# Optimization experiments

Hardware: AMD Instinct MI355X
Metric: run time of the kernel (lower is better)

The kernel has to match this reference:

```python
import jax, jax.numpy as jnp
import numpy as np

N = 50000      # nodes
E = 800000     # edges
IN = 128       # in_channels
C = 32         # hidden_channels per head
H = 8          # heads
NC = 2         # num_classes
EPS = 1e-5     # batchnorm eps
SLOPE = 0.2    # leaky relu negative slope


def setup_inputs() -> dict:
    key = jax.random.key(0)
    ks = jax.random.split(key, 16)
    d = {}
    d["x"] = jax.random.normal(ks[0], (N, IN), dtype=jnp.float32)
    d["edge_index"] = jax.random.randint(ks[1], (2, E), 0, N, dtype=jnp.int64)
    # layer 0: IN -> H*C (concat)
    s0 = 1.0 / np.sqrt(IN)
    d["Wl0"] = jax.random.normal(ks[2], (IN, H * C), dtype=jnp.float32) * s0
    d["Wr0"] = jax.random.normal(ks[3], (IN, H * C), dtype=jnp.float32) * s0
    d["att0"] = jax.random.normal(ks[4], (H, C), dtype=jnp.float32) * (1.0 / np.sqrt(C))
    d["b0"] = jnp.zeros((H * C,), dtype=jnp.float32)
    d["g0"] = jnp.ones((H * C,), dtype=jnp.float32)
    d["be0"] = jnp.zeros((H * C,), dtype=jnp.float32)
    d["m0"] = jax.random.normal(ks[5], (H * C,), dtype=jnp.float32) * 0.1
    d["v0"] = jax.random.uniform(ks[6], (H * C,), dtype=jnp.float32, minval=0.5, maxval=1.5)
    # layer 1: H*C -> C (mean over heads, concat=False)
    s1 = 1.0 / np.sqrt(H * C)
    d["Wl1"] = jax.random.normal(ks[7], (H * C, H * C), dtype=jnp.float32) * s1
    d["Wr1"] = jax.random.normal(ks[8], (H * C, H * C), dtype=jnp.float32) * s1
    d["att1"] = jax.random.normal(ks[9], (H, C), dtype=jnp.float32) * (1.0 / np.sqrt(C))
    d["b1"] = jnp.zeros((C,), dtype=jnp.float32)
    d["g1"] = jnp.ones((C,), dtype=jnp.float32)
    d["be1"] = jnp.zeros((C,), dtype=jnp.float32)
    d["m1"] = jax.random.normal(ks[10], (C,), dtype=jnp.float32) * 0.1
    d["v1"] = jax.random.uniform(ks[11], (C,), dtype=jnp.float32, minval=0.5, maxval=1.5)
    # classifier C -> NC
    d["Wc"] = jax.random.normal(ks[12], (C, NC), dtype=jnp.float32) * (1.0 / np.sqrt(C))
    d["bc"] = jnp.zeros((NC,), dtype=jnp.float32)
    return d


def _gatv2_layer(x, src, dst, Wl, Wr, att, b, concat, num_nodes):
    # GATv2Conv (PyG semantics): x_l = source proj, x_r = target proj,
    # e_ij = att . LeakyReLU(x_l[j] + x_r[i]); softmax over incoming edges of i;
    # out_i = sum_j alpha_ij * x_l[j]. Self-loops are added (PyG default).
    nH, nC = att.shape
    xl = (x @ Wl).reshape(num_nodes, nH, nC)
    xr = (x @ Wr).reshape(num_nodes, nH, nC)
    e = xl[src] + xr[dst]                              # [E', H, C]
    e = jnp.where(e > 0, e, SLOPE * e)
    logits = jnp.einsum('ehc,hc->eh', e, att)          # [E', H]
    m = jax.ops.segment_max(logits, dst, num_segments=num_nodes)   # [N, H]
    ex = jnp.exp(logits - m[dst])
    denom = jax.ops.segment_sum(ex, dst, num_segments=num_nodes)   # [N, H]
    alpha = ex / denom[dst]                            # [E', H]
    msg = alpha[:, :, None] * xl[src]                  # [E', H, C]
    out = jax.ops.segment_sum(msg, dst, num_segments=num_nodes)    # [N, H, C]
    if concat:
        return out.reshape(num_nodes, nH * nC) + b
    return out.mean(axis=1) + b


def _bn(x, g, be, m, v):
    return (x - m) * jax.lax.rsqrt(v + EPS) * g + be


def reference(x, edge_index, Wl0, Wr0, att0, b0, g0, be0, m0, v0,
              Wl1, Wr1, att1, b1, g1, be1, m1, v1, Wc, bc):
    num_nodes = x.shape[0]
    loop = jnp.arange(num_nodes, dtype=edge_index.dtype)
    src = jnp.concatenate([edge_index[0], loop])
    dst = jnp.concatenate([edge_index[1], loop])
    h = _gatv2_layer(x, src, dst, Wl0, Wr0, att0, b0, True, num_nodes)
    h = _bn(h, g0, be0, m0, v0)
    h = jax.nn.elu(h)   # eval mode: dropout is identity
    h = _gatv2_layer(h, src, dst, Wl1, Wr1, att1, b1, False, num_nodes)
    h = _bn(h, g1, be1, m1, v1)
    return h @ Wc + bc
```

## Files before the change

kernel.cpp:

```cpp
#include <hip/hip_runtime.h>
#include <math.h>

#define N_NODES 50000
#define M_PAD   50048
#define E_EDGES 800000
#define IN_CH   128
#define C_CH    32
#define H_HEADS 8
#define HC      256
#define BN_EPS  1e-5f
#define SLOPE   0.2f
#define LOG2E   1.44269504f

#define SCAN_CHUNK 512
#define SCAN_B     ((N_NODES + SCAN_CHUNK - 1) / SCAN_CHUNK)

typedef _Float16 f16x8 __attribute__((ext_vector_type(8)));
typedef _Float16 f16x4 __attribute__((ext_vector_type(4)));
typedef _Float16 f16x2 __attribute__((ext_vector_type(2)));
typedef float    f32x4 __attribute__((ext_vector_type(4)));

#if __has_builtin(__builtin_amdgcn_exp2f)
#define EXP2F(x) __builtin_amdgcn_exp2f(x)
#else
#define EXP2F(x) exp2f(x)
#endif


__global__ void k_hist(const int* __restrict__ dst, int* deg, int e) {
    int i = blockIdx.x * blockDim.x + threadIdx.x;
    if (i < e) atomicAdd(&deg[dst[i]], 1);
}

__global__ __launch_bounds__(256) void k_scan_local(
        const int* __restrict__ deg, int* __restrict__ row_ptr,
        int* __restrict__ partials, int n) {
    __shared__ int sm[256];
    int t = threadIdx.x;
    int base = blockIdx.x * SCAN_CHUNK;
    int i0 = base + 2 * t, i1 = i0 + 1;
    int a = (i0 < n) ? deg[i0] : 0;
    int b = (i1 < n) ? deg[i1] : 0;
    int s = a + b;
    sm[t] = s;
    __syncthreads();
    #pragma unroll
    for (int off = 1; off < 256; off <<= 1) {
        int u = (t >= off) ? sm[t - off] : 0;
        __syncthreads();
        sm[t] += u;
        __syncthreads();
    }
    int excl = sm[t] - s;
    if (i0 < n) row_ptr[i0] = excl;
    if (i1 < n) row_ptr[i1] = excl + a;
    if (t == 255) partials[blockIdx.x] = sm[255];
}

__global__ __launch_bounds__(128) void k_scan_part(
        int* __restrict__ partials, int* __restrict__ row_ptr_n) {
    __shared__ int sm[128];
    int t = threadIdx.x;
    int v = (t < SCAN_B) ? partials[t] : 0;
    sm[t] = v;
    __syncthreads();
    #pragma unroll
    for (int off = 1; off < 128; off <<= 1) {
        int u = (t >= off) ? sm[t - off] : 0;
        __syncthreads();
        sm[t] += u;
        __syncthreads();
    }
    if (t < SCAN_B) partials[t] = sm[t] - v;
    if (t == 127) *row_ptr_n = sm[127];
}

__global__ void k_scan_add(int* __restrict__ row_ptr, int* __restrict__ cursor,
                           const int* __restrict__ partials, int n) {
    int i = blockIdx.x * blockDim.x + threadIdx.x;
    if (i < n) {
        int v = row_ptr[i] + partials[i / SCAN_CHUNK];
        row_ptr[i] = v;
        cursor[i] = v;
    }
}

__global__ void k_fill(const int* __restrict__ src, const int* __restrict__ dst,
                       int* cursor, int* csr_src, int e, int n) {
    int i = blockIdx.x * blockDim.x + threadIdx.x;
    if (i < e) {
        int d = dst[i];
        int p = atomicAdd(&cursor[d], 1);
        csr_src[p] = src[i] << 9;
    } else if (i < e + n) {
        int v = i - e;
        int p = atomicAdd(&cursor[v], 1);
        csr_src[p] = v << 9;
    }
}


__global__ void k_split_w4(const float* __restrict__ Wl0, const float* __restrict__ Wr0,
                           const float* __restrict__ Wl1, const float* __restrict__ Wr1,
                           _Float16* __restrict__ W0lt, _Float16* __restrict__ W0rt,
                           _Float16* __restrict__ W1lt, _Float16* __restrict__ W1rt,
                           int* __restrict__ deg) {
    int t = blockIdx.x * blockDim.x + threadIdx.x;
    const float* W; _Float16* O; int K, rel;
    if (t < 32768)       { W = Wl0; O = W0lt; K = 128; rel = t; }
    else if (t < 65536)  { W = Wr0; O = W0rt; K = 128; rel = t - 32768; }
    else if (t < 131072) { W = Wl1; O = W1lt; K = 256; rel = t - 65536; }
    else if (t < 196608) { W = Wr1; O = W1rt; K = 256; rel = t - 131072; }
    else { int i = t - 196608; if (i < N_NODES) deg[i] = 1; return; }
    int n = rel / K, k = rel - n * K;
    O[rel] = (_Float16)W[(size_t)k * 256 + n];
}


#define BK  32
#define LDA 40
#define CP  136

__device__ __forceinline__ f16x8 cvt_h8(float4 a, float4 b) {
    f16x8 v = { (_Float16)a.x, (_Float16)a.y, (_Float16)a.z, (_Float16)a.w,
                (_Float16)b.x, (_Float16)b.y, (_Float16)b.z, (_Float16)b.w };
    return v;
}

__global__ __launch_bounds__(512) void k_gemm_mfma(
        const _Float16* __restrict__ A16, const float* __restrict__ A32,
        const _Float16* __restrict__ W0t, const _Float16* __restrict__ W1t,
        _Float16* __restrict__ C0, _Float16* __restrict__ C1, int K) {
    __shared__ _Float16 smem[128 * CP];
    _Float16* As  = smem;
    _Float16* Bs0 = smem + 5120;
    _Float16* Bs1 = smem + 10240;
    int t = threadIdx.x;
    int lane = t & 63, wv = t >> 6;
    int quad = lane >> 4, r16 = lane & 15;
    int wm = wv >> 2;
    int wn = wv & 3;
    size_t mBase = (size_t)blockIdx.x * 128;
    size_t nBase = (size_t)blockIdx.y * 128;
    int sr = t >> 2;
    int sc = (t & 3) * 8;
    size_t rA = mBase + sr;
    const bool aValid = rA < N_NODES;
    f32x4 acc0[4][2] = {}, acc1[4][2] = {};
    f16x8 pa, pb0, pb1;
    if (A32) {
        float4 a0 = {0.f, 0.f, 0.f, 0.f}, a1 = a0;
        if (aValid) {
            const float* g = A32 + rA * K + sc;
            a0 = ((const float4*)g)[0];
            a1 = ((const float4*)g)[1];
        }
        pa = cvt_h8(a0, a1);
    } else {
        pa = *(const f16x8*)(A16 + rA * K + sc);
    }
    pb0 = *(const f16x8*)(W0t + (size_t)(nBase + sr) * K + sc);
    pb1 = *(const f16x8*)(W1t + (size_t)(nBase + sr) * K + sc);
    for (int k0 = 0; k0 < K; k0 += BK) {
        *(f16x8*)&As[sr * LDA + sc]  = pa;
        *(f16x8*)&Bs0[sr * LDA + sc] = pb0;
        *(f16x8*)&Bs1[sr * LDA + sc] = pb1;
        __syncthreads();
        int kn = k0 + BK;
        if (kn < K) {
            if (A32) {
                float4 a0 = {0.f, 0.f, 0.f, 0.f}, a1 = a0;
                if (aValid) {
                    const float* g = A32 + rA * K + kn + sc;
                    a0 = ((const float4*)g)[0];
                    a1 = ((const float4*)g)[1];
                }
                pa = cvt_h8(a0, a1);
            } else {
                pa = *(const f16x8*)(A16 + rA * K + kn + sc);
            }
            pb0 = *(const f16x8*)(W0t + (size_t)(nBase + sr) * K + kn + sc);
            pb1 = *(const f16x8*)(W1t + (size_t)(nBase + sr) * K + kn + sc);
        }
        f16x8 av[4];
        #pragma unroll
        for (int mi = 0; mi < 4; ++mi)
            av[mi] = *(f16x8*)&As[(wm * 64 + mi * 16 + r16) * LDA + quad * 8];
        #pragma unroll
        for (int ni = 0; ni < 2; ++ni) {
            f16x8 bv0 = *(f16x8*)&Bs0[(wn * 32 + ni * 16 + r16) * LDA + quad * 8];
            f16x8 bv1 = *(f16x8*)&Bs1[(wn * 32 + ni * 16 + r16) * LDA + quad * 8];
            #pragma unroll
            for (int mi = 0; mi < 4; ++mi) {
                acc0[mi][ni] = __builtin_amdgcn_mfma_f32_16x16x32_f16(av[mi], bv0, acc0[mi][ni], 0, 0, 0);
                acc1[mi][ni] = __builtin_amdgcn_mfma_f32_16x16x32_f16(av[mi], bv1, acc1[mi][ni], 0, 0, 0);
            }
        }
        __syncthreads();
    }
    int erow = t >> 2;
    int ec = (t & 3) * 8;
    size_t obase = (mBase + erow) * 256 + nBase + ec;
    #pragma unroll
    for (int tab = 0; tab < 2; ++tab) {
        __syncthreads();
        #pragma unroll
        for (int mi = 0; mi < 4; ++mi)
            #pragma unroll
            for (int ni = 0; ni < 2; ++ni)
                #pragma unroll
                for (int r = 0; r < 4; ++r) {
                    float v = tab ? acc1[mi][ni][r] : acc0[mi][ni][r];
                    smem[(wm * 64 + mi * 16 + quad * 4 + r) * CP + wn * 32 + ni * 16 + r16]
                        = (_Float16)v;
                }
        __syncthreads();
        f16x8 v0 = *(const f16x8*)&smem[erow * CP + ec];
        f16x8 v1 = *(const f16x8*)&smem[erow * CP + ec + 32];
        f16x8 v2 = *(const f16x8*)&smem[erow * CP + ec + 64];
        f16x8 v3 = *(const f16x8*)&smem[erow * CP + ec + 96];
        _Float16* C = tab ? C1 : C0;
        *(f16x8*)(C + obase)      = v0;
        *(f16x8*)(C + obase + 32) = v1;
        *(f16x8*)(C + obase + 64) = v2;
        *(f16x8*)(C + obase + 96) = v3;
    }
}


__device__ __forceinline__ float qreduce8(float p) {
    p += __builtin_bit_cast(float, __builtin_amdgcn_mov_dpp(
             __builtin_bit_cast(int, p), 0xB1, 0xF, 0xF, true));
    p += __builtin_bit_cast(float, __builtin_amdgcn_mov_dpp(
             __builtin_bit_cast(int, p), 0x4E, 0xF, 0xF, true));
    p += __shfl_xor(p, 4);
    return p;
}

__device__ __forceinline__ float edge_w16(f16x4 h, f16x4 xr, f16x4 att) {
    f16x4 e = h + xr;
    f16x4 es = e * (_Float16)SLOPE;
    f16x4 l = __builtin_elementwise_max(e, es);
#if __has_builtin(__builtin_amdgcn_fdot2)
    f16x2 l01 = __builtin_shufflevector(l, l, 0, 1);
    f16x2 l23 = __builtin_shufflevector(l, l, 2, 3);
    f16x2 a01 = __builtin_shufflevector(att, att, 0, 1);
    f16x2 a23 = __builtin_shufflevector(att, att, 2, 3);
    float p = __builtin_amdgcn_fdot2(l01, a01, 0.f, false);
    p = __builtin_amdgcn_fdot2(l23, a23, p, false);
#else
    float p = (float)l[0] * (float)att[0];
    p = fmaf((float)l[1], (float)att[1], p);
    p = fmaf((float)l[2], (float)att[2], p);
    p = fmaf((float)l[3], (float)att[3], p);
#endif
    return EXP2F(qreduce8(p));
}

__device__ __forceinline__ void acc1e(float4& acc, f16x4 h, float w) {
    acc.x = fmaf((float)h[0], w, acc.x); acc.y = fmaf((float)h[1], w, acc.y);
    acc.z = fmaf((float)h[2], w, acc.z); acc.w = fmaf((float)h[3], w, acc.w);
}

__device__ __forceinline__ float4 edge_accum(
        const char* __restrict__ xlb, f16x4 xr_h, f16x4 att_h,
        const int* __restrict__ csr_src, int beg, int end) {
    float4 acc = {0.f, 0.f, 0.f, 0.f};
    float S = 0.f;
    int j = beg;
    for (; j + 8 <= end; j += 8) {
        int o0 = csr_src[j];     int o1 = csr_src[j + 1];
        int o2 = csr_src[j + 2]; int o3 = csr_src[j + 3];
        int o4 = csr_src[j + 4]; int o5 = csr_src[j + 5];
        int o6 = csr_src[j + 6]; int o7 = csr_src[j + 7];
        f16x4 h0 = *(const f16x4*)(xlb + o0);
        f16x4 h1 = *(const f16x4*)(xlb + o1);
        f16x4 h2 = *(const f16x4*)(xlb + o2);
        f16x4 h3 = *(const f16x4*)(xlb + o3);
        f16x4 h4 = *(const f16x4*)(xlb + o4);
        f16x4 h5 = *(const f16x4*)(xlb + o5);
        f16x4 h6 = *(const f16x4*)(xlb + o6);
        f16x4 h7 = *(const f16x4*)(xlb + o7);
        float w0 = edge_w16(h0, xr_h, att_h);
        float w1 = edge_w16(h1, xr_h, att_h);
        float w2 = edge_w16(h2, xr_h, att_h);
        float w3 = edge_w16(h3, xr_h, att_h);
        float w4 = edge_w16(h4, xr_h, att_h);
        float w5 = edge_w16(h5, xr_h, att_h);
        float w6 = edge_w16(h6, xr_h, att_h);
        float w7 = edge_w16(h7, xr_h, att_h);
        S += ((w0 + w1) + (w2 + w3)) + ((w4 + w5) + (w6 + w7));
        acc1e(acc, h0, w0); acc1e(acc, h1, w1);
        acc1e(acc, h2, w2); acc1e(acc, h3, w3);
        acc1e(acc, h4, w4); acc1e(acc, h5, w5);
        acc1e(acc, h6, w6); acc1e(acc, h7, w7);
    }
    for (; j + 4 <= end; j += 4) {
        int o0 = csr_src[j];     int o1 = csr_src[j + 1];
        int o2 = csr_src[j + 2]; int o3 = csr_src[j + 3];
        f16x4 h0 = *(const f16x4*)(xlb + o0);
        f16x4 h1 = *(const f16x4*)(xlb + o1);
        f16x4 h2 = *(const f16x4*)(xlb + o2);
        f16x4 h3 = *(const f16x4*)(xlb + o3);
        float w0 = edge_w16(h0, xr_h, att_h);
        float w1 = edge_w16(h1, xr_h, att_h);
        float w2 = edge_w16(h2, xr_h, att_h);
        float w3 = edge_w16(h3, xr_h, att_h);
        S += (w0 + w1) + (w2 + w3);
        acc1e(acc, h0, w0); acc1e(acc, h1, w1);
        acc1e(acc, h2, w2); acc1e(acc, h3, w3);
    }
    for (; j < end; ++j) {
        int o = csr_src[j];
        f16x4 hv = *(const f16x4*)(xlb + o);
        float w = edge_w16(hv, xr_h, att_h);
        S += w;
        acc1e(acc, hv, w);
    }
    float inv = 1.f / S;
    acc.x *= inv; acc.y *= inv; acc.z *= inv; acc.w *= inv;
    return acc;
}

__global__ __launch_bounds__(128) void k_edge0(
        const _Float16* __restrict__ xl, const _Float16* __restrict__ xr,
        const float* __restrict__ att,
        const int* __restrict__ row_ptr, const int* __restrict__ csr_src,
        const float* __restrict__ b0, const float* __restrict__ g0,
        const float* __restrict__ be0, const float* __restrict__ m0,
        const float* __restrict__ v0,
        _Float16* __restrict__ h0) {
    int lane = threadIdx.x & 63;
    int i = __builtin_amdgcn_readfirstlane(blockIdx.x * 2 + (threadIdx.x >> 6));
    const char* xlb = (const char*)xl + lane * 8;
    f16x4 xr_h = ((const f16x4*)xr)[(size_t)i * 64 + lane];
    float4 af = ((const float4*)att)[lane];
    f16x4 att_h = { (_Float16)(af.x * LOG2E), (_Float16)(af.y * LOG2E),
                    (_Float16)(af.z * LOG2E), (_Float16)(af.w * LOG2E) };
    int beg = row_ptr[i], end = row_ptr[i + 1];
    float4 r = edge_accum(xlb, xr_h, att_h, csr_src, beg, end);
    float4 bb = ((const float4*)b0)[lane];
    float4 gg = ((const float4*)g0)[lane];
    float4 ee = ((const float4*)be0)[lane];
    float4 mm = ((const float4*)m0)[lane];
    float4 vv = ((const float4*)v0)[lane];
    float4 o;
    o.x = (r.x + bb.x - mm.x) * rsqrtf(vv.x + BN_EPS) * gg.x + ee.x;
    o.y = (r.y + bb.y - mm.y) * rsqrtf(vv.y + BN_EPS) * gg.y + ee.y;
    o.z = (r.z + bb.z - mm.z) * rsqrtf(vv.z + BN_EPS) * gg.z + ee.z;
    o.w = (r.w + bb.w - mm.w) * rsqrtf(vv.w + BN_EPS) * gg.w + ee.w;
    o.x = o.x > 0.f ? o.x : expm1f(o.x);
    o.y = o.y > 0.f ? o.y : expm1f(o.y);
    o.z = o.z > 0.f ? o.z : expm1f(o.z);
    o.w = o.w > 0.f ? o.w : expm1f(o.w);
    f16x4 hh = { (_Float16)o.x, (_Float16)o.y, (_Float16)o.z, (_Float16)o.w };
    ((f16x4*)h0)[(size_t)i * 64 + lane] = hh;
}

__global__ __launch_bounds__(128) void k_edge1(
        const _Float16* __restrict__ xl, const _Float16* __restrict__ xr,
        const float* __restrict__ att,
        const int* __restrict__ row_ptr, const int* __restrict__ csr_src,
        const float* __restrict__ b1, const float* __restrict__ g1,
        const float* __restrict__ be1, const float* __restrict__ m1,
        const float* __restrict__ v1,
        const float* __restrict__ Wc, const float* __restrict__ bc,
        float* __restrict__ out) {
    int lane = threadIdx.x & 63;
    int q = lane & 7;
    int i = __builtin_amdgcn_readfirstlane(blockIdx.x * 2 + (threadIdx.x >> 6));
    const char* xlb = (const char*)xl + lane * 8;
    f16x4 xr_h = ((const f16x4*)xr)[(size_t)i * 64 + lane];
    float4 af = ((const float4*)att)[lane];
    f16x4 att_h = { (_Float16)(af.x * LOG2E), (_Float16)(af.y * LOG2E),
                    (_Float16)(af.z * LOG2E), (_Float16)(af.w * LOG2E) };
    int beg = row_ptr[i], end = row_ptr[i + 1];
    float4 r = edge_accum(xlb, xr_h, att_h, csr_src, beg, end);
    #pragma unroll
    for (int mask = 8; mask <= 32; mask <<= 1) {
        r.x += __shfl_xor(r.x, mask);
        r.y += __shfl_xor(r.y, mask);
        r.z += __shfl_xor(r.z, mask);
        r.w += __shfl_xor(r.w, mask);
    }
    float4 bb = ((const float4*)b1)[q];
    float4 gg = ((const float4*)g1)[q];
    float4 ee = ((const float4*)be1)[q];
    float4 mm = ((const float4*)m1)[q];
    float4 vv = ((const float4*)v1)[q];
    r.x = (r.x * 0.125f + bb.x - mm.x) * rsqrtf(vv.x + BN_EPS) * gg.x + ee.x;
    r.y = (r.y * 0.125f + bb.y - mm.y) * rsqrtf(vv.y + BN_EPS) * gg.y + ee.y;
    r.z = (r.z * 0.125f + bb.z - mm.z) * rsqrtf(vv.z + BN_EPS) * gg.z + ee.z;
    r.w = (r.w * 0.125f + bb.w - mm.w) * rsqrtf(vv.w + BN_EPS) * gg.w + ee.w;
    float4 wc0 = ((const float4*)Wc)[q * 2];
    float4 wc1 = ((const float4*)Wc)[q * 2 + 1];
    float o0 = r.x * wc0.x + r.y * wc0.z + r.z * wc1.x + r.w * wc1.z;
    float o1 = r.x * wc0.y + r.y * wc0.w + r.z * wc1.y + r.w * wc1.w;
    #pragma unroll
    for (int mask = 1; mask <= 4; mask <<= 1) {
        o0 += __shfl_xor(o0, mask);
        o1 += __shfl_xor(o1, mask);
    }
    if (lane == 0) {
        float2 ov = {o0 + bc[0], o1 + bc[1]};
        *(float2*)(out + (size_t)i * 2) = ov;
    }
}


extern "C" void kernel_launch(void* const* d_in, const int* in_sizes, int n_in,
                              void* d_out, int out_size, void* d_ws, size_t ws_size,
                              hipStream_t stream) {
    const float* x    = (const float*)d_in[0];
    const int*   ei   = (const int*)d_in[1];
    const float* Wl0  = (const float*)d_in[2];
    const float* Wr0  = (const float*)d_in[3];
    const float* att0 = (const float*)d_in[4];
    const float* b0   = (const float*)d_in[5];
    const float* g0   = (const float*)d_in[6];
    const float* be0  = (const float*)d_in[7];
    const float* m0   = (const float*)d_in[8];
    const float* v0   = (const float*)d_in[9];
    const float* Wl1  = (const float*)d_in[10];
    const float* Wr1  = (const float*)d_in[11];
    const float* att1 = (const float*)d_in[12];
    const float* b1   = (const float*)d_in[13];
    const float* g1   = (const float*)d_in[14];
    const float* be1  = (const float*)d_in[15];
    const float* m1   = (const float*)d_in[16];
    const float* v1   = (const float*)d_in[17];
    const float* Wc   = (const float*)d_in[18];
    const float* bc   = (const float*)d_in[19];
    float* out = (float*)d_out;

    const int N = N_NODES, E = E_EDGES;
    const int* srcp = ei;
    const int* dstp = ei + E;

    char* p = (char*)d_ws;
    _Float16* xlf = (_Float16*)p; p += (size_t)M_PAD * HC * 2;
    _Float16* xrf = (_Float16*)p; p += (size_t)M_PAD * HC * 2;
    _Float16* h0  = (_Float16*)p; p += (size_t)M_PAD * HC * 2;
    _Float16* W0lt = (_Float16*)p; p += (size_t)HC * IN_CH * 2;
    _Float16* W0rt = (_Float16*)p; p += (size_t)HC * IN_CH * 2;
    _Float16* W1lt = (_Float16*)p; p += (size_t)HC * HC * 2;
    _Float16* W1rt = (_Float16*)p; p += (size_t)HC * HC * 2;
    int* deg      = (int*)p;
    int* row_ptr  = deg + N;
    int* cursor   = row_ptr + (N + 1);
    int* partials = cursor + N;
    int* csr_src  = partials + ((SCAN_B + 3) & ~3);

    k_split_w4<<<964, 256, 0, stream>>>(Wl0, Wr0, Wl1, Wr1,
                                        W0lt, W0rt, W1lt, W1rt, deg);
    k_hist<<<(E + 255) / 256, 256, 0, stream>>>(dstp, deg, E);
    k_scan_local<<<SCAN_B, 256, 0, stream>>>(deg, row_ptr, partials, N);
    k_scan_part<<<1, 128, 0, stream>>>(partials, row_ptr + N);
    k_scan_add<<<(N + 255) / 256, 256, 0, stream>>>(row_ptr, cursor, partials, N);
    k_fill<<<(E + N + 255) / 256, 256, 0, stream>>>(srcp, dstp, cursor, csr_src, E, N);

    dim3 ggrid(M_PAD / 128, 2);
    k_gemm_mfma<<<ggrid, 512, 0, stream>>>(nullptr, x, W0lt, W0rt, xlf, xrf, IN_CH);
    k_edge0<<<N / 2, 128, 0, stream>>>(xlf, xrf, att0, row_ptr, csr_src,
                                       b0, g0, be0, m0, v0, h0);
    k_gemm_mfma<<<ggrid, 512, 0, stream>>>(h0, nullptr, W1lt, W1rt, xlf, xrf, HC);
    k_edge1<<<N / 2, 128, 0, stream>>>(xlf, xrf, att1, row_ptr, csr_src,
                                       b1, g1, be1, m1, v1, Wc, bc, out);
}
```

Measured before the change: 380.0 us.

## Fuse CSR build stages into fewer launches and precompute BN/attention constants

The degree histogram moves into an extra grid row of the first GEMM launch, so it runs alongside the matrix work. The separate partials scan is folded into the local scan through a last-block-done atomic. Self-loop entries are written directly in scan_add instead of through atomics in fill. BatchNorm scale/shift and the log2e-scaled fp16 attention vectors are precomputed once in the weight-split kernel, which simplifies the edge-kernel epilogues. This cuts several kernel launches and some per-node recomputation, at the cost of a hipMemsetAsync, a serialized last-block scan, and histogram atomics competing with GEMM blocks.

```diff
diff --git a/kernel.cpp b/kernel.cpp
--- a/kernel.cpp
+++ b/kernel.cpp
@@ -27,20 +27,16 @@
 #endif
 
 
-__global__ void k_hist(const int* __restrict__ dst, int* deg, int e) {
-    int i = blockIdx.x * blockDim.x + threadIdx.x;
-    if (i < e) atomicAdd(&deg[dst[i]], 1);
-}
-
 __global__ __launch_bounds__(256) void k_scan_local(
         const int* __restrict__ deg, int* __restrict__ row_ptr,
-        int* __restrict__ partials, int n) {
+        int* __restrict__ partials, int* __restrict__ done, int n) {
     __shared__ int sm[256];
+    __shared__ int isLast;
     int t = threadIdx.x;
     int base = blockIdx.x * SCAN_CHUNK;
     int i0 = base + 2 * t, i1 = i0 + 1;
-    int a = (i0 < n) ? deg[i0] : 0;
-    int b = (i1 < n) ? deg[i1] : 0;
+    int a = (i0 < n) ? deg[i0] + 1 : 0;
+    int b = (i1 < n) ? deg[i1] + 1 : 0;
     int s = a + b;
     sm[t] = s;
     __syncthreads();
@@ -54,48 +50,50 @@
     int excl = sm[t] - s;
     if (i0 < n) row_ptr[i0] = excl;
     if (i1 < n) row_ptr[i1] = excl + a;
-    if (t == 255) partials[blockIdx.x] = sm[255];
-}
-
-__global__ __launch_bounds__(128) void k_scan_part(
-        int* __restrict__ partials, int* __restrict__ row_ptr_n) {
-    __shared__ int sm[128];
-    int t = threadIdx.x;
-    int v = (t < SCAN_B) ? partials[t] : 0;
-    sm[t] = v;
+    if (t == 255) {
+        partials[blockIdx.x] = sm[255];
+        __threadfence();
+        int r = atomicAdd(done, 1);
+        isLast = (r == SCAN_B - 1);
+    }
     __syncthreads();
-    #pragma unroll
-    for (int off = 1; off < 128; off <<= 1) {
-        int u = (t >= off) ? sm[t - off] : 0;
-        __syncthreads();
-        sm[t] += u;
-        __syncthreads();
-    }
-    if (t < SCAN_B) partials[t] = sm[t] - v;
-    if (t == 127) *row_ptr_n = sm[127];
+    if (isLast) {
+        __threadfence();
+        int v = (t < SCAN_B) ? partials[t] : 0;
+        __syncthreads();
+        sm[t] = v;
+        __syncthreads();
+        #pragma unroll
+        for (int off = 1; off < 256; off <<= 1) {
+            int u = (t >= off) ? sm[t - off] : 0;
+            __syncthreads();
+            sm[t] += u;
+            __syncthreads();
+        }
+        if (t < SCAN_B) partials[t] = sm[t] - v;
+        if (t == 255) row_ptr[n] = sm[255];
+    }
 }
 
 __global__ void k_scan_add(int* __restrict__ row_ptr, int* __restrict__ cursor,
+                           int* __restrict__ csr_src,
                            const int* __restrict__ partials, int n) {
     int i = blockIdx.x * blockDim.x + threadIdx.x;
     if (i < n) {
         int v = row_ptr[i] + partials[i / SCAN_CHUNK];
         row_ptr[i] = v;
-        cursor[i] = v;
+        cursor[i] = v + 1;
+        csr_src[v] = i << 9;
     }
 }
 
 __global__ void k_fill(const int* __restrict__ src, const int* __restrict__ dst,
-                       int* cursor, int* csr_src, int e, int n) {
+                       int* cursor, int* csr_src, int e) {
     int i = blockIdx.x * blockDim.x + threadIdx.x;
     if (i < e) {
         int d = dst[i];
         int p = atomicAdd(&cursor[d], 1);
         csr_src[p] = src[i] << 9;
-    } else if (i < e + n) {
-        int v = i - e;
-        int p = atomicAdd(&cursor[v], 1);
-        csr_src[p] = v << 9;
     }
 }
 
@@ -104,14 +102,38 @@
                            const float* __restrict__ Wl1, const float* __restrict__ Wr1,
                            _Float16* __restrict__ W0lt, _Float16* __restrict__ W0rt,
                            _Float16* __restrict__ W1lt, _Float16* __restrict__ W1rt,
-                           int* __restrict__ deg) {
+                           const float* __restrict__ att0, const float* __restrict__ att1,
+                           const float* __restrict__ b0, const float* __restrict__ g0,
+                           const float* __restrict__ be0, const float* __restrict__ m0,
+                           const float* __restrict__ v0,
+                           const float* __restrict__ b1, const float* __restrict__ g1,
+                           const float* __restrict__ be1, const float* __restrict__ m1,
+                           const float* __restrict__ v1,
+                           float* __restrict__ sc0, float* __restrict__ sh0,
+                           float* __restrict__ sc1, float* __restrict__ sh1,
+                           _Float16* __restrict__ attl0, _Float16* __restrict__ attl1) {
     int t = blockIdx.x * blockDim.x + threadIdx.x;
     const float* W; _Float16* O; int K, rel;
     if (t < 32768)       { W = Wl0; O = W0lt; K = 128; rel = t; }
     else if (t < 65536)  { W = Wr0; O = W0rt; K = 128; rel = t - 32768; }
     else if (t < 131072) { W = Wl1; O = W1lt; K = 256; rel = t - 65536; }
     else if (t < 196608) { W = Wr1; O = W1rt; K = 256; rel = t - 131072; }
-    else { int i = t - 196608; if (i < N_NODES) deg[i] = 1; return; }
+    else {
+        int ch = t - 196608;
+        if (ch < 256) {
+            float s = rsqrtf(v0[ch] + BN_EPS) * g0[ch];
+            sc0[ch] = s;
+            sh0[ch] = (b0[ch] - m0[ch]) * s + be0[ch];
+            attl0[ch] = (_Float16)(att0[ch] * LOG2E);
+            attl1[ch] = (_Float16)(att1[ch] * LOG2E);
+            if (ch < 32) {
+                float s1 = rsqrtf(v1[ch] + BN_EPS) * g1[ch];
+                sc1[ch] = 0.125f * s1;
+                sh1[ch] = (b1[ch] - m1[ch]) * s1 + be1[ch];
+            }
+        }
+        return;
+    }
     int n = rel / K, k = rel - n * K;
     O[rel] = (_Float16)W[(size_t)k * 256 + n];
 }
@@ -130,7 +152,15 @@
 __global__ __launch_bounds__(512) void k_gemm_mfma(
         const _Float16* __restrict__ A16, const float* __restrict__ A32,
         const _Float16* __restrict__ W0t, const _Float16* __restrict__ W1t,
-        _Float16* __restrict__ C0, _Float16* __restrict__ C1, int K) {
+        _Float16* __restrict__ C0, _Float16* __restrict__ C1, int K,
+        const int* __restrict__ hdst, int* __restrict__ hdeg, int he) {
+    if (blockIdx.y == 2) {
+        int tid = blockIdx.x * blockDim.x + threadIdx.x;
+        int stride = gridDim.x * blockDim.x;
+        for (int i = tid; i < he; i += stride)
+            atomicAdd(&hdeg[hdst[i]], 1);
+        return;
+    }
     __shared__ _Float16 smem[128 * CP];
     _Float16* As  = smem;
     _Float16* Bs0 = smem + 5120;
@@ -324,31 +354,24 @@
 
 __global__ __launch_bounds__(128) void k_edge0(
         const _Float16* __restrict__ xl, const _Float16* __restrict__ xr,
-        const float* __restrict__ att,
+        const _Float16* __restrict__ attl,
         const int* __restrict__ row_ptr, const int* __restrict__ csr_src,
-        const float* __restrict__ b0, const float* __restrict__ g0,
-        const float* __restrict__ be0, const float* __restrict__ m0,
-        const float* __restrict__ v0,
+        const float* __restrict__ sc0, const float* __restrict__ sh0,
         _Float16* __restrict__ h0) {
     int lane = threadIdx.x & 63;
     int i = __builtin_amdgcn_readfirstlane(blockIdx.x * 2 + (threadIdx.x >> 6));
     const char* xlb = (const char*)xl + lane * 8;
     f16x4 xr_h = ((const f16x4*)xr)[(size_t)i * 64 + lane];
-    float4 af = ((const float4*)att)[lane];
-    f16x4 att_h = { (_Float16)(af.x * LOG2E), (_Float16)(af.y * LOG2E),
-                    (_Float16)(af.z * LOG2E), (_Float16)(af.w * LOG2E) };
+    f16x4 att_h = ((const f16x4*)attl)[lane];
     int beg = row_ptr[i], end = row_ptr[i + 1];
     float4 r = edge_accum(xlb, xr_h, att_h, csr_src, beg, end);
-    float4 bb = ((const float4*)b0)[lane];
-    float4 gg = ((const float4*)g0)[lane];
-    float4 ee = ((const float4*)be0)[lane];
-    float4 mm = ((const float4*)m0)[lane];
-    float4 vv = ((const float4*)v0)[lane];
+    float4 sc = ((const float4*)sc0)[lane];
+    float4 sh = ((const float4*)sh0)[lane];
     float4 o;
-    o.x = (r.x + bb.x - mm.x) * rsqrtf(vv.x + BN_EPS) * gg.x + ee.x;
-    o.y = (r.y + bb.y - mm.y) * rsqrtf(vv.y + BN_EPS) * gg.y + ee.y;
-    o.z = (r.z + bb.z - mm.z) * rsqrtf(vv.z + BN_EPS) * gg.z + ee.z;
-    o.w = (r.w + bb.w - mm.w) * rsqrtf(vv.w + BN_EPS) * gg.w + ee.w;
+    o.x = r.x * sc.x + sh.x;
+    o.y = r.y * sc.y + sh.y;
+    o.z = r.z * sc.z + sh.z;
+    o.w = r.w * sc.w + sh.w;
     o.x = o.x > 0.f ? o.x : expm1f(o.x);
     o.y = o.y > 0.f ? o.y : expm1f(o.y);
     o.z = o.z > 0.f ? o.z : expm1f(o.z);
@@ -359,11 +382,9 @@
 
 __global__ __launch_bounds__(128) void k_edge1(
         const _Float16* __restrict__ xl, const _Float16* __restrict__ xr,
-        const float* __restrict__ att,
+        const _Float16* __restrict__ attl,
         const int* __restrict__ row_ptr, const int* __restrict__ csr_src,
-        const float* __restrict__ b1, const float* __restrict__ g1,
-        const float* __restrict__ be1, const float* __restrict__ m1,
-        const float* __restrict__ v1,
+        const float* __restrict__ sc1, const float* __restrict__ sh1,
         const float* __restrict__ Wc, const float* __restrict__ bc,
         float* __restrict__ out) {
     int lane = threadIdx.x & 63;
@@ -371,9 +392,7 @@
     int i = __builtin_amdgcn_readfirstlane(blockIdx.x * 2 + (threadIdx.x >> 6));
     const char* xlb = (const char*)xl + lane * 8;
     f16x4 xr_h = ((const f16x4*)xr)[(size_t)i * 64 + lane];
-    float4 af = ((const float4*)att)[lane];
-    f16x4 att_h = { (_Float16)(af.x * LOG2E), (_Float16)(af.y * LOG2E),
-                    (_Float16)(af.z * LOG2E), (_Float16)(af.w * LOG2E) };
+    f16x4 att_h = ((const f16x4*)attl)[lane];
     int beg = row_ptr[i], end = row_ptr[i + 1];
     float4 r = edge_accum(xlb, xr_h, att_h, csr_src, beg, end);
     #pragma unroll
@@ -383,15 +402,12 @@
         r.z += __shfl_xor(r.z, mask);
         r.w += __shfl_xor(r.w, mask);
     }
-    float4 bb = ((const float4*)b1)[q];
-    float4 gg = ((const float4*)g1)[q];
-    float4 ee = ((const float4*)be1)[q];
-    float4 mm = ((const float4*)m1)[q];
-    float4 vv = ((const float4*)v1)[q];
-    r.x = (r.x * 0.125f + bb.x - mm.x) * rsqrtf(vv.x + BN_EPS) * gg.x + ee.x;
-    r.y = (r.y * 0.125f + bb.y - mm.y) * rsqrtf(vv.y + BN_EPS) * gg.y + ee.y;
-    r.z = (r.z * 0.125f + bb.z - mm.z) * rsqrtf(vv.z + BN_EPS) * gg.z + ee.z;
-    r.w = (r.w * 0.125f + bb.w - mm.w) * rsqrtf(vv.w + BN_EPS) * gg.w + ee.w;
+    float4 sA = ((const float4*)sc1)[q];
+    float4 sB = ((const float4*)sh1)[q];
+    r.x = r.x * sA.x + sB.x;
+    r.y = r.y * sA.y + sB.y;
+    r.z = r.z * sA.z + sB.z;
+    r.w = r.w * sA.w + sB.w;
     float4 wc0 = ((const float4*)Wc)[q * 2];
     float4 wc1 = ((const float4*)Wc)[q * 2 + 1];
     float o0 = r.x * wc0.x + r.y * wc0.z + r.z * wc1.x + r.w * wc1.z;
@@ -445,25 +461,42 @@
     _Float16* W0rt = (_Float16*)p; p += (size_t)HC * IN_CH * 2;
     _Float16* W1lt = (_Float16*)p; p += (size_t)HC * HC * 2;
     _Float16* W1rt = (_Float16*)p; p += (size_t)HC * HC * 2;
+    float* sc0 = (float*)p;       p += 256 * 4;
+    float* sh0 = (float*)p;       p += 256 * 4;
+    float* sc1 = (float*)p;       p += 32 * 4;
+    float* sh1 = (float*)p;       p += 32 * 4;
+    _Float16* attl0 = (_Float16*)p; p += 256 * 2;
+    _Float16* attl1 = (_Float16*)p; p += 256 * 2;
     int* deg      = (int*)p;
-    int* row_ptr  = deg + N;
+    int* done     = deg + N;
+    int* row_ptr  = done + 4;
     int* cursor   = row_ptr + (N + 1);
     int* partials = cursor + N;
-    int* csr_src  = partials + ((SCAN_B + 3) & ~3);
-
-    k_split_w4<<<964, 256, 0, stream>>>(Wl0, Wr0, Wl1, Wr1,
-                                        W0lt, W0rt, W1lt, W1rt, deg);
-    k_hist<<<(E + 255) / 256, 256, 0, stream>>>(dstp, deg, E);
-    k_scan_local<<<SCAN_B, 256, 0, stream>>>(deg, row_ptr, partials, N);
-    k_scan_part<<<1, 128, 0, stream>>>(partials, row_ptr + N);
-    k_scan_add<<<(N + 255) / 256, 256, 0, stream>>>(row_ptr, cursor, partials, N);
-    k_fill<<<(E + N + 255) / 256, 256, 0, stream>>>(srcp, dstp, cursor, csr_src, E, N);
-
-    dim3 ggrid(M_PAD / 128, 2);
-    k_gemm_mfma<<<ggrid, 512, 0, stream>>>(nullptr, x, W0lt, W0rt, xlf, xrf, IN_CH);
-    k_edge0<<<N / 2, 128, 0, stream>>>(xlf, xrf, att0, row_ptr, csr_src,
-                                       b0, g0, be0, m0, v0, h0);
-    k_gemm_mfma<<<ggrid, 512, 0, stream>>>(h0, nullptr, W1lt, W1rt, xlf, xrf, HC);
-    k_edge1<<<N / 2, 128, 0, stream>>>(xlf, xrf, att1, row_ptr, csr_src,
-                                       b1, g1, be1, m1, v1, Wc, bc, out);
-}
+    int* csr_src  = partials + 104;
+
+    hipMemsetAsync(deg, 0, (size_t)(N + 4) * sizeof(int), stream);
+
+    k_split_w4<<<769, 256, 0, stream>>>(Wl0, Wr0, Wl1, Wr1,
+                                        W0lt, W0rt, W1lt, W1rt,
+                                        att0, att1,
+                                        b0, g0, be0, m0, v0,
+                                        b1, g1, be1, m1, v1,
+                                        sc0, sh0, sc1, sh1, attl0, attl1);
+
+    dim3 ggrid0(M_PAD / 128, 3);
+    k_gemm_mfma<<<ggrid0, 512, 0, stream>>>(nullptr, x, W0lt, W0rt, xlf, xrf,
+                                            IN_CH, dstp, deg, E);
+
+    k_scan_local<<<SCAN_B, 256, 0, stream>>>(deg, row_ptr, partials, done, N);
+    k_scan_add<<<(N + 255) / 256, 256, 0, stream>>>(row_ptr, cursor, csr_src,
+                                                    partials, N);
+    k_fill<<<(E + 255) / 256, 256, 0, stream>>>(srcp, dstp, cursor, csr_src, E);
+
+    k_edge0<<<N / 2, 128, 0, stream>>>(xlf, xrf, attl0, row_ptr, csr_src,
+                                       sc0, sh0, h0);
+    dim3 ggrid1(M_PAD / 128, 2);
+    k_gemm_mfma<<<ggrid1, 512, 0, stream>>>(h0, nullptr, W1lt, W1rt, xlf, xrf,
+                                            HC, nullptr, nullptr, 0);
+    k_edge1<<<N / 2, 128, 0, stream>>>(xlf, xrf, attl1, row_ptr, csr_src,
+                                       sc1, sh1, Wc, bc, out);
+}
```

New measurement: 357.5 us. 1.06x faster.
